# Kernel tuning notes

Hardware: AMD Instinct MI355X
Metric: run time of the kernel (lower is better)

The kernel has to match this reference:

```python
import jax, jax.numpy as jnp
import numpy as np

N_NODES = 50000
N_EDGES = 300000
NODE_DIM = 11
EDGE_DIM = 5
HID = 256
L = 4
G = 1024  # num graphs
BN_EPS = 1e-5


def setup_inputs() -> dict:
    key = jax.random.key(0)
    ks = jax.random.split(key, 24)
    s = 0.05
    inp = {
        "x": jax.random.normal(ks[0], (N_NODES, NODE_DIM), jnp.float32),
        "edge_index": jax.random.randint(ks[1], (2, N_EDGES), 0, N_NODES, jnp.int32),
        "edge_attr": jax.random.normal(ks[2], (N_EDGES, EDGE_DIM), jnp.float32),
        "batch": jnp.sort(jax.random.randint(ks[3], (N_NODES,), 0, G, jnp.int32)),
        # node encoder
        "enc_W": jax.random.normal(ks[4], (NODE_DIM, HID), jnp.float32) * s,
        "enc_b": jnp.zeros((HID,), jnp.float32),
        # per-layer GINE params (stacked over layers)
        "edge_W": jax.random.normal(ks[5], (L, EDGE_DIM, HID), jnp.float32) * s,
        "edge_b": jnp.zeros((L, HID), jnp.float32),
        "mlp_W1": jax.random.normal(ks[6], (L, HID, HID), jnp.float32) * s,
        "mlp_b1": jnp.zeros((L, HID), jnp.float32),
        "mlp_W2": jax.random.normal(ks[7], (L, HID, HID), jnp.float32) * s,
        "mlp_b2": jnp.zeros((L, HID), jnp.float32),
        "bn_g": jnp.ones((L, HID), jnp.float32),
        "bn_b": jnp.zeros((L, HID), jnp.float32),
        # head: 3*HID -> HID -> HID//2 -> 1
        "head_W1": jax.random.normal(ks[8], (3 * HID, HID), jnp.float32) * s,
        "head_b1": jnp.zeros((HID,), jnp.float32),
        "head_W2": jax.random.normal(ks[9], (HID, HID // 2), jnp.float32) * s,
        "head_b2": jnp.zeros((HID // 2,), jnp.float32),
        "head_W3": jax.random.normal(ks[10], (HID // 2, 1), jnp.float32) * s,
        "head_b3": jnp.zeros((1,), jnp.float32),
    }
    return inp


def _forward(x, edge_attr, enc_W, enc_b, edge_W, edge_b, mlp_W1, mlp_b1,
             mlp_W2, mlp_b2, bn_g, bn_b, head_W1, head_b1, head_W2, head_b2,
             head_W3, head_b3, edge_index, batch):
    n = x.shape[0]
    src, dst = edge_index[0], edge_index[1]  # messages flow src(j) -> dst(i)
    h = jax.nn.relu(x @ enc_W + enc_b)  # [N, HID]
    for l in range(L):
        e = edge_attr @ edge_W[l] + edge_b[l]                 # [E, HID]
        msg = jax.nn.relu(h[src] + e)                         # [E, HID]
        aggr = jax.ops.segment_sum(msg, dst, num_segments=n)  # [N, HID]
        z = h + aggr                                          # (1+eps)*h + aggr, eps=0
        z = jax.nn.relu(z @ mlp_W1[l] + mlp_b1[l]) @ mlp_W2[l] + mlp_b2[l]
        # BatchNorm over node dim (batch statistics)
        mu = jnp.mean(z, axis=0)
        var = jnp.var(z, axis=0)
        z = (z - mu) * jax.lax.rsqrt(var + BN_EPS) * bn_g[l] + bn_b[l]
        h = jax.nn.relu(z) + h  # residual
    # mean / add / max pooling per graph
    sums = jax.ops.segment_sum(h, batch, num_segments=G)      # [G, HID]
    cnt = jax.ops.segment_sum(jnp.ones((n, 1), h.dtype), batch, num_segments=G)
    mean = sums / jnp.maximum(cnt, 1.0)
    mx = jax.ops.segment_max(h, batch, num_segments=G)
    g = jnp.concatenate([mean, sums, mx], axis=1)             # [G, 3*HID]
    g = jax.nn.relu(g @ head_W1 + head_b1)
    g = jax.nn.relu(g @ head_W2 + head_b2)
    out = g @ head_W3 + head_b3
    return out.reshape(-1)  # [G]


def reference(x, edge_index, edge_attr, batch, enc_W, enc_b, edge_W, edge_b,
              mlp_W1, mlp_b1, mlp_W2, mlp_b2, bn_g, bn_b, head_W1, head_b1,
              head_W2, head_b2, head_W3, head_b3):
    return _forward(x, edge_attr, enc_W, enc_b, edge_W, edge_b, mlp_W1, mlp_b1,
                    mlp_W2, mlp_b2, bn_g, bn_b, head_W1, head_b1, head_W2,
                    head_b2, head_W3, head_b3, edge_index, batch)
```

## Files before the change

### kernel.cpp

```cpp
#include <hip/hip_runtime.h>

#define N_NODES 50000
#define N_EDGES 300000
#define G_GRAPHS 1024
#define HID 256
#define NLAYERS 4

typedef unsigned short ushort_t;
typedef __attribute__((ext_vector_type(8))) short bf16x8;
typedef __attribute__((ext_vector_type(8))) unsigned short u16x8;
typedef __attribute__((ext_vector_type(4))) float f32x4;

__device__ __forceinline__ float bf2f(ushort_t u) {
  unsigned int x = ((unsigned int)u) << 16;
  return __builtin_bit_cast(float, x);
}
__device__ __forceinline__ ushort_t f2bf(float f) {
  unsigned int x = __builtin_bit_cast(unsigned int, f);
  unsigned int lsb = (x >> 16) & 1u;
  x += 0x7fffu + lsb;
  return (ushort_t)(x >> 16);
}

__global__ __launch_bounds__(256) void k_encoder(const float* __restrict__ x,
    const float* __restrict__ W, const float* __restrict__ b,
    ushort_t* __restrict__ h, int n)
{
  int j = threadIdx.x;
  float wcol[11];
#pragma unroll
  for (int k = 0; k < 11; ++k) wcol[k] = W[k * HID + j];
  float bj = b[j];
  __shared__ float xs[8][11];
  int base = blockIdx.x * 8;
  if (j < 88) {
    int r = j / 11, k = j % 11;
    int row = base + r;
    if (row < n) xs[r][k] = x[row * 11 + k];
  }
  __syncthreads();
#pragma unroll
  for (int r = 0; r < 8; ++r) {
    int row = base + r;
    if (row >= n) break;
    float acc = bj;
#pragma unroll
    for (int k = 0; k < 11; ++k) acc += xs[r][k] * wcol[k];
    h[(size_t)row * HID + j] = f2bf(fmaxf(acc, 0.f));
  }
}

__global__ __launch_bounds__(256) void k_hist(const int* __restrict__ dst,
    int* __restrict__ offs, int E)
{
  int e = blockIdx.x * 256 + threadIdx.x;
  if (e < E) atomicAdd(&offs[dst[e]], 1);
}

__global__ __launch_bounds__(1024) void k_scanA(int* __restrict__ offs,
    int* __restrict__ btot, int n)
{
  __shared__ int wsum[16];
  int tid = threadIdx.x, lane = tid & 63, wid = tid >> 6;
  int idx = blockIdx.x * 1024 + tid;
  int v = (idx < n) ? offs[idx] : 0;
  int x = v;
#pragma unroll
  for (int off = 1; off < 64; off <<= 1) {
    int t = __shfl_up(x, off);
    if (lane >= off) x += t;
  }
  if (lane == 63) wsum[wid] = x;
  __syncthreads();
  if (wid == 0 && lane < 16) {
    int w = wsum[lane];
#pragma unroll
    for (int off = 1; off < 16; off <<= 1) {
      int t = __shfl_up(w, off);
      if (lane >= off) w += t;
    }
    wsum[lane] = w;
  }
  __syncthreads();
  int wbase = (wid == 0) ? 0 : wsum[wid - 1];
  if (idx < n) offs[idx] = wbase + x - v;
  if (tid == 0) btot[blockIdx.x] = wsum[15];
}

__global__ __launch_bounds__(1024) void k_scanC(int* __restrict__ offs,
    const int* __restrict__ btot, int n)
{
  __shared__ int sbase;
  if (threadIdx.x == 0) {
    int s = 0;
    for (int i = 0; i < blockIdx.x; ++i) s += btot[i];
    sbase = s;
  }
  __syncthreads();
  int idx = blockIdx.x * 1024 + threadIdx.x;
  if (idx < n) offs[idx] += sbase;
}

__global__ __launch_bounds__(256) void k_fill(const int* __restrict__ src,
    const int* __restrict__ dst, int* __restrict__ offs,
    int* __restrict__ esrc, ushort_t* __restrict__ eab,
    const float* __restrict__ ea, int E)
{
  int e = blockIdx.x * 256 + threadIdx.x;
  if (e < E) {
    int d = dst[e];
    int p = atomicAdd(&offs[d], 1);
    esrc[p] = src[e];
    const float* ep = ea + (size_t)e * 5;
    ushort4 lo = make_ushort4(f2bf(ep[0]), f2bf(ep[1]), f2bf(ep[2]), f2bf(ep[3]));
    ushort4 hi = make_ushort4(f2bf(ep[4]), 0, 0, 0);
    *(ushort4*)&eab[(size_t)p * 8] = lo;
    *(ushort4*)&eab[(size_t)p * 8 + 4] = hi;
  }
}

__global__ __launch_bounds__(256) void k_prep(const float* __restrict__ W1,
    const float* __restrict__ W2, ushort_t* __restrict__ Wt1,
    ushort_t* __restrict__ Wt2)
{
  __shared__ float ld[16][257];
  int mat = blockIdx.y & (NLAYERS - 1);
  int which = blockIdx.y >> 2;
  const float* Wm = (which ? W2 : W1) + (size_t)mat * HID * HID;
  ushort_t* Wtm = (which ? Wt2 : Wt1) + (size_t)mat * HID * HID;
  int k0 = blockIdx.x * 16;
  int tid = threadIdx.x;
#pragma unroll
  for (int i = 0; i < 16; ++i) ld[i][tid] = Wm[(size_t)(k0 + i) * HID + tid];
  __syncthreads();
#pragma unroll
  for (int v = 0; v < 4; ++v) {
    ushort4 u = make_ushort4(f2bf(ld[v*4+0][tid]), f2bf(ld[v*4+1][tid]),
                             f2bf(ld[v*4+2][tid]), f2bf(ld[v*4+3][tid]));
    *(ushort4*)&Wtm[(size_t)tid * HID + k0 + v * 4] = u;
  }
}

__global__ __launch_bounds__(256) void k_prept(const float* __restrict__ W,
    ushort_t* __restrict__ Wt, int K, int N)
{
  int idx = blockIdx.x * 256 + threadIdx.x;
  if (idx >= K * N) return;
  int n = idx / K, k = idx % K;
  Wt[idx] = f2bf(W[(size_t)k * N + n]);
}

struct ev5 { ushort_t s0, s1, s2, s3, s4; };

__device__ __forceinline__ void edge_step(ev5 ev, ushort4 hv,
    const float4& w0, const float4& w1, const float4& w2, const float4& w3,
    const float4& w4, const float4& bi,
    float& ax, float& ay, float& az, float& aw)
{
  float v0 = bf2f(ev.s0), v1 = bf2f(ev.s1), v2 = bf2f(ev.s2),
        v3 = bf2f(ev.s3), v4 = bf2f(ev.s4);
  float m0 = bi.x, m1 = bi.y, m2 = bi.z, m3 = bi.w;
  m0 = fmaf(v0, w0.x, m0); m1 = fmaf(v0, w0.y, m1);
  m2 = fmaf(v0, w0.z, m2); m3 = fmaf(v0, w0.w, m3);
  m0 = fmaf(v1, w1.x, m0); m1 = fmaf(v1, w1.y, m1);
  m2 = fmaf(v1, w1.z, m2); m3 = fmaf(v1, w1.w, m3);
  m0 = fmaf(v2, w2.x, m0); m1 = fmaf(v2, w2.y, m1);
  m2 = fmaf(v2, w2.z, m2); m3 = fmaf(v2, w2.w, m3);
  m0 = fmaf(v3, w3.x, m0); m1 = fmaf(v3, w3.y, m1);
  m2 = fmaf(v3, w3.z, m2); m3 = fmaf(v3, w3.w, m3);
  m0 = fmaf(v4, w4.x, m0); m1 = fmaf(v4, w4.y, m1);
  m2 = fmaf(v4, w4.z, m2); m3 = fmaf(v4, w4.w, m3);
  m0 += bf2f(hv.x); m1 += bf2f(hv.y); m2 += bf2f(hv.z); m3 += bf2f(hv.w);
  ax += fmaxf(m0, 0.f); ay += fmaxf(m1, 0.f);
  az += fmaxf(m2, 0.f); aw += fmaxf(m3, 0.f);
}

__global__ __launch_bounds__(256) void k_gather(const ushort_t* __restrict__ h,
    const int* __restrict__ offs, const int* __restrict__ esrc,
    const ushort_t* __restrict__ eab, const float* __restrict__ eW,
    const float* __restrict__ eb, ushort_t* __restrict__ zin,
    float* __restrict__ stats, int n)
{
  int tid = threadIdx.x;
  if (blockIdx.x == 0) { stats[tid] = 0.f; stats[HID + tid] = 0.f; }
  int wave = tid >> 6, lane = tid & 63;
  int node = blockIdx.x * 4 + wave;
  int c4 = lane * 4;
  float4 w0 = *(const float4*)&eW[0 * HID + c4];
  float4 w1 = *(const float4*)&eW[1 * HID + c4];
  float4 w2 = *(const float4*)&eW[2 * HID + c4];
  float4 w3 = *(const float4*)&eW[3 * HID + c4];
  float4 w4 = *(const float4*)&eW[4 * HID + c4];
  float4 bi = *(const float4*)&eb[c4];
  if (node >= n) return;
  int lo = (node == 0) ? 0 : offs[node - 1];
  int hi = offs[node];
  ushort4 ho = *(const ushort4*)&h[(size_t)node * HID + c4];
  float ax = bf2f(ho.x), ay = bf2f(ho.y), az = bf2f(ho.z), aw = bf2f(ho.w);
  int p = lo;
  for (; p + 3 < hi; p += 4) {
    int s0 = esrc[p], s1 = esrc[p + 1], s2 = esrc[p + 2], s3 = esrc[p + 3];
    ev5 ea0 = *(const ev5*)&eab[(size_t)(p + 0) * 8];
    ev5 ea1 = *(const ev5*)&eab[(size_t)(p + 1) * 8];
    ev5 ea2 = *(const ev5*)&eab[(size_t)(p + 2) * 8];
    ev5 ea3 = *(const ev5*)&eab[(size_t)(p + 3) * 8];
    ushort4 h0 = *(const ushort4*)&h[(size_t)s0 * HID + c4];
    ushort4 h1 = *(const ushort4*)&h[(size_t)s1 * HID + c4];
    ushort4 h2 = *(const ushort4*)&h[(size_t)s2 * HID + c4];
    ushort4 h3 = *(const ushort4*)&h[(size_t)s3 * HID + c4];
    edge_step(ea0, h0, w0, w1, w2, w3, w4, bi, ax, ay, az, aw);
    edge_step(ea1, h1, w0, w1, w2, w3, w4, bi, ax, ay, az, aw);
    edge_step(ea2, h2, w0, w1, w2, w3, w4, bi, ax, ay, az, aw);
    edge_step(ea3, h3, w0, w1, w2, w3, w4, bi, ax, ay, az, aw);
  }
  for (; p < hi; ++p) {
    int s0 = esrc[p];
    ev5 ea0 = *(const ev5*)&eab[(size_t)p * 8];
    ushort4 h0 = *(const ushort4*)&h[(size_t)s0 * HID + c4];
    edge_step(ea0, h0, w0, w1, w2, w3, w4, bi, ax, ay, az, aw);
  }
  *(ushort4*)&zin[(size_t)node * HID + c4] =
      make_ushort4(f2bf(ax), f2bf(ay), f2bf(az), f2bf(aw));
}

__global__ __launch_bounds__(512, 1) void k_mlp(const ushort_t* __restrict__ A,
    const ushort_t* __restrict__ Wt1, const float* __restrict__ b1,
    const ushort_t* __restrict__ Wt2, const float* __restrict__ b2,
    ushort_t* __restrict__ out, float* __restrict__ stats, int M)
{
  __shared__ alignas(16) ushort_t w2L[65536];
  __shared__ alignas(16) ushort_t z1s[2][16 * 264];
  int tid = threadIdx.x;
  int wave = tid >> 6, lane = tid & 63;
  int m = lane & 15, quad = lane >> 4;
  int col0 = wave * 32;
  for (int c = tid; c < 8192; c += 512) {
    int f = c >> 6, l = c & 63;
    int ctg = f >> 3, kt = f & 7;
    int n = ctg * 16 + (l & 15);
    int k = kt * 32 + (l >> 4) * 8;
    *(u16x8*)&w2L[f * 512 + l * 8] = *(const u16x8*)(Wt2 + (size_t)n * HID + k);
  }
  bf16x8 w1f[2][8];
#pragma unroll
  for (int ct = 0; ct < 2; ++ct)
#pragma unroll
    for (int kt = 0; kt < 8; ++kt)
      w1f[ct][kt] = *(const bf16x8*)(
          Wt1 + (size_t)(col0 + ct * 16 + m) * HID + kt * 32 + quad * 8);
  float bv1[2] = {b1[col0 + m], b1[col0 + 16 + m]};
  float bv2[2] = {b2[col0 + m], b2[col0 + 16 + m]};
  float csum[2] = {0.f, 0.f}, csq[2] = {0.f, 0.f};
  int ntiles = M >> 4;
  int parity = 0;
  int ctg0 = wave * 2, ctg1 = wave * 2 + 1;
  __syncthreads();
  int t = blockIdx.x;
  bf16x8 af[8];
  if (t < ntiles) {
    const ushort_t* Ap = A + (size_t)(t * 16 + m) * HID + quad * 8;
#pragma unroll
    for (int kt = 0; kt < 8; ++kt) af[kt] = *(const bf16x8*)(Ap + kt * 32);
  }
  for (; t < ntiles; t += gridDim.x) {
    int tn = t + gridDim.x;
    int tcl = (tn < ntiles) ? tn : t;
    const ushort_t* Apn = A + (size_t)(tcl * 16 + m) * HID + quad * 8;
    bf16x8 afn[8];
#pragma unroll
    for (int kt = 0; kt < 8; ++kt) afn[kt] = *(const bf16x8*)(Apn + kt * 32);
    f32x4 a0 = (f32x4){0.f, 0.f, 0.f, 0.f};
    f32x4 a1 = (f32x4){0.f, 0.f, 0.f, 0.f};
#pragma unroll
    for (int kt = 0; kt < 8; ++kt) {
      a0 = __builtin_amdgcn_mfma_f32_16x16x32_bf16(af[kt], w1f[0][kt], a0, 0, 0, 0);
      a1 = __builtin_amdgcn_mfma_f32_16x16x32_bf16(af[kt], w1f[1][kt], a1, 0, 0, 0);
    }
    ushort_t* buf = z1s[parity];
#pragma unroll
    for (int reg = 0; reg < 4; ++reg) {
      int r = quad * 4 + reg;
      buf[r * 264 + col0 + m]      = f2bf(fmaxf(a0[reg] + bv1[0], 0.f));
      buf[r * 264 + col0 + 16 + m] = f2bf(fmaxf(a1[reg] + bv1[1], 0.f));
    }
    __syncthreads();
    f32x4 c0 = (f32x4){0.f, 0.f, 0.f, 0.f};
    f32x4 c1 = (f32x4){0.f, 0.f, 0.f, 0.f};
#pragma unroll
    for (int kt = 0; kt < 8; ++kt) {
      bf16x8 zf = *(const bf16x8*)&buf[m * 264 + kt * 32 + quad * 8];
      bf16x8 b0 = *(const bf16x8*)&w2L[(ctg0 * 8 + kt) * 512 + lane * 8];
      bf16x8 b1r = *(const bf16x8*)&w2L[(ctg1 * 8 + kt) * 512 + lane * 8];
      c0 = __builtin_amdgcn_mfma_f32_16x16x32_bf16(zf, b0, c0, 0, 0, 0);
      c1 = __builtin_amdgcn_mfma_f32_16x16x32_bf16(zf, b1r, c1, 0, 0, 0);
    }
    int rb = t * 16 + quad * 4;
#pragma unroll
    for (int reg = 0; reg < 4; ++reg) {
      float o0 = c0[reg] + bv2[0];
      float o1 = c1[reg] + bv2[1];
      out[(size_t)(rb + reg) * HID + col0 + m] = f2bf(o0);
      out[(size_t)(rb + reg) * HID + col0 + 16 + m] = f2bf(o1);
      csum[0] += o0; csq[0] = fmaf(o0, o0, csq[0]);
      csum[1] += o1; csq[1] = fmaf(o1, o1, csq[1]);
    }
#pragma unroll
    for (int kt = 0; kt < 8; ++kt) af[kt] = afn[kt];
    parity ^= 1;
  }
#pragma unroll
  for (int ct = 0; ct < 2; ++ct) {
    float s = csum[ct], q = csq[ct];
    s += __shfl_xor(s, 16); s += __shfl_xor(s, 32);
    q += __shfl_xor(q, 16); q += __shfl_xor(q, 32);
    if (quad == 0) {
      unsafeAtomicAdd(&stats[col0 + ct * 16 + m], s);
      unsafeAtomicAdd(&stats[HID + col0 + ct * 16 + m], q);
    }
  }
}

__global__ __launch_bounds__(256) void k_bn_apply(const ushort_t* __restrict__ z,
    const float* __restrict__ stats, const float* __restrict__ g,
    const float* __restrict__ b, ushort_t* __restrict__ h, int total4)
{
  int idx = blockIdx.x * 256 + threadIdx.x;
  if (idx >= total4) return;
  int col = (idx & 63) * 4;
  const float inv_n = 1.f / (float)N_NODES;
  float sc[4], sh[4];
#pragma unroll
  for (int c = 0; c < 4; ++c) {
    float mu = stats[col + c] * inv_n;
    float var = stats[HID + col + c] * inv_n - mu * mu;
    float rs = rsqrtf(var + 1e-5f);
    sc[c] = g[col + c] * rs;
    sh[c] = b[col + c] - mu * sc[c];
  }
  ushort4 zv = *(const ushort4*)(z + (size_t)idx * 4);
  ushort4 hv = *(const ushort4*)(h + (size_t)idx * 4);
  float o0 = fmaxf(fmaf(bf2f(zv.x), sc[0], sh[0]), 0.f) + bf2f(hv.x);
  float o1 = fmaxf(fmaf(bf2f(zv.y), sc[1], sh[1]), 0.f) + bf2f(hv.y);
  float o2 = fmaxf(fmaf(bf2f(zv.z), sc[2], sh[2]), 0.f) + bf2f(hv.z);
  float o3 = fmaxf(fmaf(bf2f(zv.w), sc[3], sh[3]), 0.f) + bf2f(hv.w);
  *(ushort4*)(h + (size_t)idx * 4) = make_ushort4(f2bf(o0), f2bf(o1), f2bf(o2), f2bf(o3));
}

__device__ __forceinline__ int lbound(const int* __restrict__ b, int n, int key) {
  int lo = 0, hi = n;
  while (lo < hi) {
    int mid = (lo + hi) >> 1;
    if (b[mid] < key) lo = mid + 1; else hi = mid;
  }
  return lo;
}

__global__ __launch_bounds__(256) void k_pool_bn(const ushort_t* __restrict__ z,
    const float* __restrict__ stats, const float* __restrict__ g_,
    const float* __restrict__ b_, const ushort_t* __restrict__ h,
    const int* __restrict__ batch, ushort_t* __restrict__ gf)
{
  int g = blockIdx.x, j = threadIdx.x;
  const float inv_n = 1.f / (float)N_NODES;
  float mu = stats[j] * inv_n;
  float var = stats[HID + j] * inv_n - mu * mu;
  float rs = rsqrtf(var + 1e-5f);
  float sc = g_[j] * rs;
  float sh = b_[j] - mu * sc;
  int lo = lbound(batch, N_NODES, g);
  int hi = lbound(batch, N_NODES, g + 1);
  float s = 0.f, mx = 0.f;
  for (int i = lo; i < hi; ++i) {
    float zv = bf2f(z[(size_t)i * HID + j]);
    float hv = bf2f(h[(size_t)i * HID + j]);
    float v = fmaxf(fmaf(zv, sc, sh), 0.f) + hv;
    s += v; mx = fmaxf(mx, v);
  }
  float cntv = fmaxf((float)(hi - lo), 1.f);
  size_t base = (size_t)g * 768;
  gf[base + j] = f2bf(s / cntv);
  gf[base + 256 + j] = f2bf(s);
  gf[base + 512 + j] = f2bf(mx);
}

template<int KT, int DO_RELU>
__global__ __launch_bounds__(256, 1) void k_head_gemm(const ushort_t* __restrict__ A,
    const ushort_t* __restrict__ Bt, const float* __restrict__ bias,
    ushort_t* __restrict__ out, int M, int N)
{
  const int K = KT * 32;
  int tid = threadIdx.x;
  int wave = tid >> 6, lane = tid & 63;
  int m = lane & 15, quad = lane >> 4;
  int col = (blockIdx.y * 4 + wave) * 16 + m;
  bf16x8 bfrag[KT];
#pragma unroll
  for (int kt = 0; kt < KT; ++kt)
    bfrag[kt] = *(const bf16x8*)(Bt + (size_t)col * K + kt * 32 + quad * 8);
  float bv = bias[col];
  int ntiles = M >> 4;
  for (int t = blockIdx.x; t < ntiles; t += gridDim.x) {
    const ushort_t* Ap = A + (size_t)(t * 16 + m) * K + quad * 8;
    bf16x8 af[KT];
#pragma unroll
    for (int kt = 0; kt < KT; ++kt) af[kt] = *(const bf16x8*)(Ap + kt * 32);
    f32x4 acc = (f32x4){0.f, 0.f, 0.f, 0.f};
#pragma unroll
    for (int kt = 0; kt < KT; ++kt)
      acc = __builtin_amdgcn_mfma_f32_16x16x32_bf16(af[kt], bfrag[kt], acc, 0, 0, 0);
    int rb = t * 16 + quad * 4;
#pragma unroll
    for (int reg = 0; reg < 4; ++reg) {
      float o = acc[reg] + bv;
      if (DO_RELU) o = fmaxf(o, 0.f);
      out[(size_t)(rb + reg) * N + col] = f2bf(o);
    }
  }
}

__global__ __launch_bounds__(256) void k_head_out(const ushort_t* __restrict__ g2,
    const float* __restrict__ W3, const float* __restrict__ b3,
    float* __restrict__ out)
{
  int wave = threadIdx.x >> 6, lane = threadIdx.x & 63;
  int g = blockIdx.x * 4 + wave;
  ushort2 v = *(const ushort2*)&g2[(size_t)g * 128 + lane * 2];
  float p = bf2f(v.x) * W3[lane * 2] + bf2f(v.y) * W3[lane * 2 + 1];
#pragma unroll
  for (int off = 32; off > 0; off >>= 1) p += __shfl_down(p, off);
  if (lane == 0) out[g] = p + b3[0];
}

extern "C" void kernel_launch(void* const* d_in, const int* in_sizes, int n_in,
                              void* d_out, int out_size, void* d_ws, size_t ws_size,
                              hipStream_t stream)
{
  const float* x     = (const float*)d_in[0];
  const int*   ei    = (const int*)d_in[1];
  const float* ea    = (const float*)d_in[2];
  const int*   batch = (const int*)d_in[3];
  const float* encW  = (const float*)d_in[4];
  const float* encB  = (const float*)d_in[5];
  const float* edgeW = (const float*)d_in[6];
  const float* edgeB = (const float*)d_in[7];
  const float* W1    = (const float*)d_in[8];
  const float* b1    = (const float*)d_in[9];
  const float* W2    = (const float*)d_in[10];
  const float* b2    = (const float*)d_in[11];
  const float* bng   = (const float*)d_in[12];
  const float* bnb   = (const float*)d_in[13];
  const float* hW1   = (const float*)d_in[14];
  const float* hb1   = (const float*)d_in[15];
  const float* hW2   = (const float*)d_in[16];
  const float* hb2   = (const float*)d_in[17];
  const float* hW3   = (const float*)d_in[18];
  const float* hb3   = (const float*)d_in[19];
  float* out = (float*)d_out;

  const size_t NH = (size_t)N_NODES * HID;
  char* base = (char*)d_ws;
  auto alloc = [&](size_t bytes) -> char* {
    char* p = base; base += (bytes + 63) & ~(size_t)63; return p;
  };
  float*    stats = (float*)alloc(512 * 4);
  int*      offs  = (int*)alloc(50001 * 4);
  int*      btot  = (int*)alloc(64 * 4);
  int*      esrc  = (int*)alloc((size_t)N_EDGES * 4);
  ushort_t* eab   = (ushort_t*)alloc((size_t)N_EDGES * 8 * 2);
  ushort_t* Wt1   = (ushort_t*)alloc((size_t)NLAYERS * HID * HID * 2);
  ushort_t* Wt2   = (ushort_t*)alloc((size_t)NLAYERS * HID * HID * 2);
  ushort_t* hW1t  = (ushort_t*)alloc((size_t)768 * 256 * 2);
  ushort_t* hW2t  = (ushort_t*)alloc((size_t)256 * 128 * 2);
  ushort_t* gf    = (ushort_t*)alloc((size_t)G_GRAPHS * 768 * 2);
  ushort_t* g1    = (ushort_t*)alloc((size_t)G_GRAPHS * 256 * 2);
  ushort_t* g2    = (ushort_t*)alloc((size_t)G_GRAPHS * 128 * 2);
  ushort_t* zin   = (ushort_t*)alloc(NH * 2);
  ushort_t* h     = (ushort_t*)alloc(NH * 2);

  const int* src = ei;
  const int* dst = ei + N_EDGES;

  hipMemsetAsync(offs, 0, 50001 * sizeof(int), stream);
  k_hist<<<(N_EDGES + 255) / 256, 256, 0, stream>>>(dst, offs, N_EDGES);
  const int NSB = (N_NODES + 1023) / 1024;
  k_scanA<<<NSB, 1024, 0, stream>>>(offs, btot, N_NODES);
  k_scanC<<<NSB, 1024, 0, stream>>>(offs, btot, N_NODES);
  k_fill<<<(N_EDGES + 255) / 256, 256, 0, stream>>>(src, dst, offs, esrc, eab, ea, N_EDGES);
  k_prep<<<dim3(16, 2 * NLAYERS), 256, 0, stream>>>(W1, W2, Wt1, Wt2);
  k_prept<<<(768 * 256 + 255) / 256, 256, 0, stream>>>(hW1, hW1t, 768, 256);
  k_prept<<<(256 * 128 + 255) / 256, 256, 0, stream>>>(hW2, hW2t, 256, 128);

  k_encoder<<<(N_NODES + 7) / 8, 256, 0, stream>>>(x, encW, encB, h, N_NODES);

  for (int l = 0; l < NLAYERS; ++l) {
    k_gather<<<N_NODES / 4, 256, 0, stream>>>(
        h, offs, esrc, eab, edgeW + (size_t)l * 5 * HID, edgeB + (size_t)l * HID,
        zin, stats, N_NODES);
    k_mlp<<<256, 512, 0, stream>>>(
        zin, Wt1 + (size_t)l * HID * HID, b1 + (size_t)l * HID,
        Wt2 + (size_t)l * HID * HID, b2 + (size_t)l * HID, zin, stats, N_NODES);
    if (l < NLAYERS - 1) {
      k_bn_apply<<<(N_NODES * HID / 4 + 255) / 256, 256, 0, stream>>>(
          zin, stats, bng + (size_t)l * HID, bnb + (size_t)l * HID, h,
          N_NODES * HID / 4);
    }
  }

  k_pool_bn<<<G_GRAPHS, 256, 0, stream>>>(
      zin, stats, bng + (size_t)(NLAYERS - 1) * HID,
      bnb + (size_t)(NLAYERS - 1) * HID, h, batch, gf);
  k_head_gemm<24, 1><<<dim3(16, 4), 256, 0, stream>>>(gf, hW1t, hb1, g1, G_GRAPHS, 256);
  k_head_gemm<8, 1><<<dim3(16, 2), 256, 0, stream>>>(g1, hW2t, hb2, g2, G_GRAPHS, 128);
  k_head_out<<<G_GRAPHS / 4, 256, 0, stream>>>(g2, hW3, hb3, out);
}
```

Before: 610.2 us.

## Split MLP kernel output columns across two blocks to raise occupancy

The fused two-layer MLP kernel now launches a 2-D grid in which each block computes half of the second GEMM's output columns. This halves the W2 LDS footprint, so more blocks can fit per CU (launch bounds raised to 4). Each block still recomputes the full first GEMM for its tile, so that work is duplicated. Output now goes to a separate z2 buffer, which avoids an in-place write hazard between the two column blocks. The register prefetch of the next A tile and the double-buffered z1 were removed and replaced by an extra barrier.

```diff
diff --git a/kernel.cpp b/kernel.cpp
--- a/kernel.cpp
+++ b/kernel.cpp
@@ -223,21 +223,22 @@
       make_ushort4(f2bf(ax), f2bf(ay), f2bf(az), f2bf(aw));
 }
 
-__global__ __launch_bounds__(512, 1) void k_mlp(const ushort_t* __restrict__ A,
+__global__ __launch_bounds__(512, 4) void k_mlp(const ushort_t* __restrict__ A,
     const ushort_t* __restrict__ Wt1, const float* __restrict__ b1,
     const ushort_t* __restrict__ Wt2, const float* __restrict__ b2,
     ushort_t* __restrict__ out, float* __restrict__ stats, int M)
 {
-  __shared__ alignas(16) ushort_t w2L[65536];
-  __shared__ alignas(16) ushort_t z1s[2][16 * 264];
+  __shared__ alignas(16) ushort_t w2L[32768];
+  __shared__ alignas(16) ushort_t z1s[16 * 264];
   int tid = threadIdx.x;
   int wave = tid >> 6, lane = tid & 63;
   int m = lane & 15, quad = lane >> 4;
+  int gy = blockIdx.y;
   int col0 = wave * 32;
-  for (int c = tid; c < 8192; c += 512) {
+  for (int c = tid; c < 4096; c += 512) {
     int f = c >> 6, l = c & 63;
     int ctg = f >> 3, kt = f & 7;
-    int n = ctg * 16 + (l & 15);
+    int n = gy * 128 + ctg * 16 + (l & 15);
     int k = kt * 32 + (l >> 4) * 8;
     *(u16x8*)&w2L[f * 512 + l * 8] = *(const u16x8*)(Wt2 + (size_t)n * HID + k);
   }
@@ -249,26 +250,16 @@
       w1f[ct][kt] = *(const bf16x8*)(
           Wt1 + (size_t)(col0 + ct * 16 + m) * HID + kt * 32 + quad * 8);
   float bv1[2] = {b1[col0 + m], b1[col0 + 16 + m]};
-  float bv2[2] = {b2[col0 + m], b2[col0 + 16 + m]};
-  float csum[2] = {0.f, 0.f}, csq[2] = {0.f, 0.f};
+  int mycol = gy * 128 + wave * 16 + m;
+  float bv2 = b2[mycol];
+  float csum = 0.f, csq = 0.f;
   int ntiles = M >> 4;
-  int parity = 0;
-  int ctg0 = wave * 2, ctg1 = wave * 2 + 1;
-  __syncthreads();
-  int t = blockIdx.x;
-  bf16x8 af[8];
-  if (t < ntiles) {
+  __syncthreads();
+  for (int t = blockIdx.x; t < ntiles; t += gridDim.x) {
     const ushort_t* Ap = A + (size_t)(t * 16 + m) * HID + quad * 8;
+    bf16x8 af[8];
 #pragma unroll
     for (int kt = 0; kt < 8; ++kt) af[kt] = *(const bf16x8*)(Ap + kt * 32);
-  }
-  for (; t < ntiles; t += gridDim.x) {
-    int tn = t + gridDim.x;
-    int tcl = (tn < ntiles) ? tn : t;
-    const ushort_t* Apn = A + (size_t)(tcl * 16 + m) * HID + quad * 8;
-    bf16x8 afn[8];
-#pragma unroll
-    for (int kt = 0; kt < 8; ++kt) afn[kt] = *(const bf16x8*)(Apn + kt * 32);
     f32x4 a0 = (f32x4){0.f, 0.f, 0.f, 0.f};
     f32x4 a1 = (f32x4){0.f, 0.f, 0.f, 0.f};
 #pragma unroll
@@ -276,47 +267,35 @@
       a0 = __builtin_amdgcn_mfma_f32_16x16x32_bf16(af[kt], w1f[0][kt], a0, 0, 0, 0);
       a1 = __builtin_amdgcn_mfma_f32_16x16x32_bf16(af[kt], w1f[1][kt], a1, 0, 0, 0);
     }
-    ushort_t* buf = z1s[parity];
+    __syncthreads();
 #pragma unroll
     for (int reg = 0; reg < 4; ++reg) {
       int r = quad * 4 + reg;
-      buf[r * 264 + col0 + m]      = f2bf(fmaxf(a0[reg] + bv1[0], 0.f));
-      buf[r * 264 + col0 + 16 + m] = f2bf(fmaxf(a1[reg] + bv1[1], 0.f));
+      z1s[r * 264 + col0 + m]      = f2bf(fmaxf(a0[reg] + bv1[0], 0.f));
+      z1s[r * 264 + col0 + 16 + m] = f2bf(fmaxf(a1[reg] + bv1[1], 0.f));
     }
     __syncthreads();
     f32x4 c0 = (f32x4){0.f, 0.f, 0.f, 0.f};
-    f32x4 c1 = (f32x4){0.f, 0.f, 0.f, 0.f};
 #pragma unroll
     for (int kt = 0; kt < 8; ++kt) {
-      bf16x8 zf = *(const bf16x8*)&buf[m * 264 + kt * 32 + quad * 8];
-      bf16x8 b0 = *(const bf16x8*)&w2L[(ctg0 * 8 + kt) * 512 + lane * 8];
-      bf16x8 b1r = *(const bf16x8*)&w2L[(ctg1 * 8 + kt) * 512 + lane * 8];
+      bf16x8 zf = *(const bf16x8*)&z1s[m * 264 + kt * 32 + quad * 8];
+      bf16x8 b0 = *(const bf16x8*)&w2L[(wave * 8 + kt) * 512 + lane * 8];
       c0 = __builtin_amdgcn_mfma_f32_16x16x32_bf16(zf, b0, c0, 0, 0, 0);
-      c1 = __builtin_amdgcn_mfma_f32_16x16x32_bf16(zf, b1r, c1, 0, 0, 0);
     }
     int rb = t * 16 + quad * 4;
 #pragma unroll
     for (int reg = 0; reg < 4; ++reg) {
-      float o0 = c0[reg] + bv2[0];
-      float o1 = c1[reg] + bv2[1];
-      out[(size_t)(rb + reg) * HID + col0 + m] = f2bf(o0);
-      out[(size_t)(rb + reg) * HID + col0 + 16 + m] = f2bf(o1);
-      csum[0] += o0; csq[0] = fmaf(o0, o0, csq[0]);
-      csum[1] += o1; csq[1] = fmaf(o1, o1, csq[1]);
-    }
-#pragma unroll
-    for (int kt = 0; kt < 8; ++kt) af[kt] = afn[kt];
-    parity ^= 1;
-  }
-#pragma unroll
-  for (int ct = 0; ct < 2; ++ct) {
-    float s = csum[ct], q = csq[ct];
-    s += __shfl_xor(s, 16); s += __shfl_xor(s, 32);
-    q += __shfl_xor(q, 16); q += __shfl_xor(q, 32);
-    if (quad == 0) {
-      unsafeAtomicAdd(&stats[col0 + ct * 16 + m], s);
-      unsafeAtomicAdd(&stats[HID + col0 + ct * 16 + m], q);
-    }
+      float o = c0[reg] + bv2;
+      out[(size_t)(rb + reg) * HID + mycol] = f2bf(o);
+      csum += o; csq = fmaf(o, o, csq);
+    }
+  }
+  float s = csum, q = csq;
+  s += __shfl_xor(s, 16); s += __shfl_xor(s, 32);
+  q += __shfl_xor(q, 16); q += __shfl_xor(q, 32);
+  if (quad == 0) {
+    unsafeAtomicAdd(&stats[mycol], s);
+    unsafeAtomicAdd(&stats[HID + mycol], q);
   }
 }
 
@@ -475,6 +454,7 @@
   ushort_t* g1    = (ushort_t*)alloc((size_t)G_GRAPHS * 256 * 2);
   ushort_t* g2    = (ushort_t*)alloc((size_t)G_GRAPHS * 128 * 2);
   ushort_t* zin   = (ushort_t*)alloc(NH * 2);
+  ushort_t* z2    = (ushort_t*)alloc(NH * 2);
   ushort_t* h     = (ushort_t*)alloc(NH * 2);
 
   const int* src = ei;
@@ -496,18 +476,18 @@
     k_gather<<<N_NODES / 4, 256, 0, stream>>>(
         h, offs, esrc, eab, edgeW + (size_t)l * 5 * HID, edgeB + (size_t)l * HID,
         zin, stats, N_NODES);
-    k_mlp<<<256, 512, 0, stream>>>(
+    k_mlp<<<dim3(256, 2), 512, 0, stream>>>(
         zin, Wt1 + (size_t)l * HID * HID, b1 + (size_t)l * HID,
-        Wt2 + (size_t)l * HID * HID, b2 + (size_t)l * HID, zin, stats, N_NODES);
+        Wt2 + (size_t)l * HID * HID, b2 + (size_t)l * HID, z2, stats, N_NODES);
     if (l < NLAYERS - 1) {
       k_bn_apply<<<(N_NODES * HID / 4 + 255) / 256, 256, 0, stream>>>(
-          zin, stats, bng + (size_t)l * HID, bnb + (size_t)l * HID, h,
+          z2, stats, bng + (size_t)l * HID, bnb + (size_t)l * HID, h,
           N_NODES * HID / 4);
     }
   }
 
   k_pool_bn<<<G_GRAPHS, 256, 0, stream>>>(
-      zin, stats, bng + (size_t)(NLAYERS - 1) * HID,
+      z2, stats, bng + (size_t)(NLAYERS - 1) * HID,
       bnb + (size_t)(NLAYERS - 1) * HID, h, batch, gf);
   k_head_gemm<24, 1><<<dim3(16, 4), 256, 0, stream>>>(gf, hW1t, hb1, g1, G_GRAPHS, 256);
   k_head_gemm<8, 1><<<dim3(16, 2), 256, 0, stream>>>(g1, hW2t, hb2, g2, G_GRAPHS, 128);
```

Result: slower. 695.2 us (+13.9%).
